# Performance work log

Hardware: AMD Instinct MI355X
Metric: run time of the kernel (lower is better)

## Reference

```python
import jax, jax.numpy as jnp
import numpy as np

N_NODES = 50000
N_EDGES = 800000
D_IN = 128
HIDDEN = 128
N_LAYERS = 3
N_CLASSES = 10
N_GRAPHS = 512
BN_EPS = 1e-5


def gcn_conv(x, edges, W, b):
    """PyG GCNConv: D^{-1/2}(A+I)D^{-1/2} X W + b (self-loops added)."""
    N = x.shape[0]
    src, dst = edges[0], edges[1]
    # degrees with self-loops
    deg = jax.ops.segment_sum(jnp.ones(src.shape[0], x.dtype), dst, num_segments=N) + 1.0
    dinv = jax.lax.rsqrt(deg)
    h = x @ W                                   # [N, out]
    norm = dinv[src] * dinv[dst]                # [E]
    out = jax.ops.segment_sum(h[src] * norm[:, None], dst, num_segments=N)
    out = out + h * (dinv * dinv)[:, None]      # self-loop messages
    return out + b


def batch_norm(x, gamma, beta):
    # BatchNorm1d in training mode: batch stats over node axis, biased var
    mu = x.mean(axis=0)
    var = x.var(axis=0)
    return gamma * (x - mu) * jax.lax.rsqrt(var + BN_EPS) + beta


def setup_inputs() -> dict:
    key = jax.random.key(0)
    ks = jax.random.split(key, 12)
    x = jax.random.normal(ks[0], (N_NODES, D_IN), dtype=jnp.float32)
    edges = jax.random.randint(ks[1], (2, N_EDGES), 0, N_NODES, dtype=jnp.int64)
    batch = jnp.sort(jax.random.randint(ks[2], (N_NODES,), 0, N_GRAPHS, dtype=jnp.int64))
    s_in = 1.0 / np.sqrt(D_IN)
    s_h = 1.0 / np.sqrt(HIDDEN)
    return {
        "x": x,
        "edges": edges,
        "batch": batch,
        "W1": jax.random.normal(ks[3], (D_IN, HIDDEN), dtype=jnp.float32) * s_in,
        "b1": jnp.zeros((HIDDEN,), jnp.float32),
        "g1": jnp.ones((HIDDEN,), jnp.float32),
        "be1": jnp.zeros((HIDDEN,), jnp.float32),
        "Wc": jax.random.normal(ks[4], (N_LAYERS, HIDDEN, HIDDEN), dtype=jnp.float32) * s_h,
        "bc": jnp.zeros((N_LAYERS, HIDDEN), jnp.float32),
        "gc": jnp.ones((N_LAYERS, HIDDEN), jnp.float32),
        "bec": jnp.zeros((N_LAYERS, HIDDEN), jnp.float32),
        "Wl": jax.random.normal(ks[5], (HIDDEN, N_CLASSES), dtype=jnp.float32) * s_h,
        "bl": jnp.zeros((N_CLASSES,), jnp.float32),
    }


def reference(x, edges, batch, W1, b1, g1, be1, Wc, bc, gc, bec, Wl, bl):
    h = jax.nn.relu(batch_norm(gcn_conv(x, edges, W1, b1), g1, be1))
    for i in range(N_LAYERS):  # fixed small layer loop
        h = jax.nn.relu(batch_norm(gcn_conv(h, edges, Wc[i], bc[i]), gc[i], bec[i]))
    # global_mean_pool over per-node graph ids
    sums = jax.ops.segment_sum(h, batch, num_segments=N_GRAPHS)
    counts = jax.ops.segment_sum(jnp.ones(h.shape[0], h.dtype), batch, num_segments=N_GRAPHS)
    pooled = sums / jnp.maximum(counts, 1.0)[:, None]
    return pooled @ Wl + bl
```

## Files before the change

### kernel.cpp

```cpp
#include <hip/hip_runtime.h>
#include <hip/hip_bf16.h>

#define NN 50000
#define NE 800000
#define DH 128
#define NGRAPH 512
#define NCLS 10
#define BN_EPS 1e-5f
#define SCAN_NB ((NN + 255) / 256)
#define GEMM_NB ((NN + 63) / 64)
#define BN1_NB 1024
#define BN2_NB 32
#define FILL_SEG 392
#define FILL_NB (FILL_SEG * 8)
#define STRIPE ((NN + 7) / 8)

typedef unsigned int uint;
typedef unsigned short ushort;
typedef __attribute__((ext_vector_type(8))) short short8;
typedef __attribute__((ext_vector_type(4))) float f32x4;

__device__ __forceinline__ ushort f2bf(float x) {
    __hip_bfloat16 h = __float2bfloat16(x);
    return *(ushort*)&h;
}
__device__ __forceinline__ float bf_lo(uint v) { return __uint_as_float(v << 16); }
__device__ __forceinline__ float bf_hi(uint v) { return __uint_as_float(v & 0xffff0000u); }


__global__ void hist_kernel(const int* __restrict__ dst, int* __restrict__ counts, int E) {
    int e = blockIdx.x * blockDim.x + threadIdx.x;
    if (e < E) atomicAdd(&counts[dst[e]], 1);
}

__global__ void compute_dinv_kernel(const int* __restrict__ counts, float* __restrict__ dinv, int N) {
    int n = blockIdx.x * blockDim.x + threadIdx.x;
    if (n < N) dinv[n] = rsqrtf((float)(counts[n] + 1));
}

__launch_bounds__(256)
__global__ void scan1_kernel(const int* __restrict__ counts, int* __restrict__ bsum, int N) {
    __shared__ int ls[256];
    int i = blockIdx.x * 256 + threadIdx.x;
    ls[threadIdx.x] = (i < N) ? counts[i] : 0;
    __syncthreads();
    for (int off = 128; off > 0; off >>= 1) {
        if (threadIdx.x < off) ls[threadIdx.x] += ls[threadIdx.x + off];
        __syncthreads();
    }
    if (threadIdx.x == 0) bsum[blockIdx.x] = ls[0];
}

__launch_bounds__(256)
__global__ void scan2_kernel(int* __restrict__ bsum, int NB) {
    __shared__ int ls[256];
    int tid = threadIdx.x;
    int v = (tid < NB) ? bsum[tid] : 0;
    ls[tid] = v;
    __syncthreads();
    for (int off = 1; off < 256; off <<= 1) {
        int t = (tid >= off) ? ls[tid - off] : 0;
        __syncthreads();
        ls[tid] += t;
        __syncthreads();
    }
    if (tid < NB) bsum[tid] = ls[tid] - v;
}

__launch_bounds__(256)
__global__ void scan3_kernel(const int* __restrict__ counts, const int* __restrict__ boff,
                             int* __restrict__ offsets, int* __restrict__ cursor, int N) {
    __shared__ int ls[256];
    int tid = threadIdx.x;
    int i = blockIdx.x * 256 + tid;
    int v = (i < N) ? counts[i] : 0;
    ls[tid] = v;
    __syncthreads();
    for (int off = 1; off < 256; off <<= 1) {
        int t = (tid >= off) ? ls[tid - off] : 0;
        __syncthreads();
        ls[tid] += t;
        __syncthreads();
    }
    int base = boff[blockIdx.x];
    if (i < N) {
        int ex = base + ls[tid] - v;
        offsets[i] = ex;
        cursor[i] = ex;
        if (i == N - 1) offsets[N] = base + ls[tid];
    }
}

__launch_bounds__(256)
__global__ void fill_kernel(const int* __restrict__ src, const int* __restrict__ dst,
                            int* __restrict__ cursor, int* __restrict__ csr_src, int E) {
    int stripe = blockIdx.x & 7;
    int seg = blockIdx.x >> 3;
    int lo = stripe * STRIPE;
    int hi = lo + STRIPE;
    for (int e = seg * 256 + threadIdx.x; e < E; e += FILL_SEG * 256) {
        int d = dst[e];
        if (d >= lo && d < hi) {
            int pos = atomicAdd(&cursor[d], 1);
            csr_src[pos] = src[e];
        }
    }
}


__launch_bounds__(256)
__global__ void wtrans_kernel(const float* __restrict__ W1, const float* __restrict__ Wc,
                              ushort* __restrict__ WT) {
    int layer = blockIdx.x >> 4;
    int kt = (blockIdx.x >> 2) & 3, nt = blockIdx.x & 3;
    const float* W = (layer == 0) ? W1 : Wc + (size_t)(layer - 1) * DH * DH;
    __shared__ float tile[32][33];
    int t = threadIdx.x;
    int r = t >> 3;
    int c4 = (t & 7) * 4;
    float4 v = *(const float4*)&W[(size_t)(kt * 32 + r) * DH + nt * 32 + c4];
    tile[r][c4 + 0] = v.x; tile[r][c4 + 1] = v.y;
    tile[r][c4 + 2] = v.z; tile[r][c4 + 3] = v.w;
    __syncthreads();
    int n = t >> 3, k4 = (t & 7) * 4;
    ushort4 o;
    o.x = f2bf(tile[k4 + 0][n]);
    o.y = f2bf(tile[k4 + 1][n]);
    o.z = f2bf(tile[k4 + 2][n]);
    o.w = f2bf(tile[k4 + 3][n]);
    *(ushort4*)&WT[(size_t)layer * DH * DH + (size_t)(nt * 32 + n) * DH + kt * 32 + k4] = o;
}


template<int MODE>
__launch_bounds__(256)
__global__ void gemm_kernel(const float* __restrict__ Xf, const uint* __restrict__ Xb,
                            const ushort* __restrict__ WTl,
                            const float* __restrict__ bnacc, const float* __restrict__ gamma,
                            const float* __restrict__ beta, const float* __restrict__ dinv,
                            ushort* __restrict__ H, int N) {
    __shared__ uint4 xs4[64 * 16];
    __shared__ uint4 wt4[128 * 16];
    int t = threadIdx.x;
    int kc = t & 15;
    int row0 = blockIdx.x * 64;

    float sc[8], sh[8];
    if (MODE) {
        const float invN = 1.0f / (float)NN;
        #pragma unroll
        for (int j = 0; j < 8; j++) {
            int f = kc * 8 + j;
            float mean = bnacc[f] * invN;
            float var = bnacc[128 + f] * invN - mean * mean;
            float s = gamma[f] * rsqrtf(var + BN_EPS);
            sc[j] = s;
            sh[j] = beta[f] - mean * s;
        }
    }

    #pragma unroll
    for (int i = 0; i < 4; i++) {
        int row = (t >> 4) + i * 16;
        int r = row0 + row;
        float v[8];
        if (r < N) {
            if (MODE) {
                uint4 raw = ((const uint4*)Xb)[(size_t)r * 16 + kc];
                v[0] = bf_lo(raw.x); v[1] = bf_hi(raw.x);
                v[2] = bf_lo(raw.y); v[3] = bf_hi(raw.y);
                v[4] = bf_lo(raw.z); v[5] = bf_hi(raw.z);
                v[6] = bf_lo(raw.w); v[7] = bf_hi(raw.w);
                #pragma unroll
                for (int j = 0; j < 8; j++) v[j] = fmaxf(v[j] * sc[j] + sh[j], 0.f);
            } else {
                float4 a = ((const float4*)Xf)[(size_t)r * 32 + kc * 2];
                float4 b = ((const float4*)Xf)[(size_t)r * 32 + kc * 2 + 1];
                v[0] = a.x; v[1] = a.y; v[2] = a.z; v[3] = a.w;
                v[4] = b.x; v[5] = b.y; v[6] = b.z; v[7] = b.w;
            }
        } else {
            #pragma unroll
            for (int j = 0; j < 8; j++) v[j] = 0.f;
        }
        uint4 p;
        p.x = (uint)f2bf(v[0]) | ((uint)f2bf(v[1]) << 16);
        p.y = (uint)f2bf(v[2]) | ((uint)f2bf(v[3]) << 16);
        p.z = (uint)f2bf(v[4]) | ((uint)f2bf(v[5]) << 16);
        p.w = (uint)f2bf(v[6]) | ((uint)f2bf(v[7]) << 16);
        xs4[row * 16 + (kc ^ (row & 7))] = p;
    }
    const uint4* WT4 = (const uint4*)WTl;
    #pragma unroll
    for (int i = 0; i < 8; i++) {
        int n = (t >> 4) + i * 16;
        wt4[n * 16 + (kc ^ (n & 7))] = WT4[n * 16 + kc];
    }
    __syncthreads();

    int w = t >> 6, l = t & 63;
    int l16 = l >> 4;
    int lrow = w * 16 + (l & 15);
    f32x4 acc[8];
    #pragma unroll
    for (int c = 0; c < 8; c++) acc[c] = (f32x4){0.f, 0.f, 0.f, 0.f};

    #pragma unroll
    for (int ks = 0; ks < 4; ks++) {
        int kk = ks * 4 + l16;
        uint4 av = xs4[lrow * 16 + (kk ^ (lrow & 7))];
        short8 a = *(short8*)&av;
        #pragma unroll
        for (int c = 0; c < 8; c++) {
            int n = c * 16 + (l & 15);
            uint4 bv = wt4[n * 16 + (kk ^ (n & 7))];
            short8 b = *(short8*)&bv;
            acc[c] = __builtin_amdgcn_mfma_f32_16x16x32_bf16(a, b, acc[c], 0, 0, 0);
        }
    }

    #pragma unroll
    for (int j = 0; j < 4; j++) {
        int grow = row0 + w * 16 + l16 * 4 + j;
        if (grow < N) {
            float dv = dinv[grow];
            #pragma unroll
            for (int c = 0; c < 8; c++) {
                H[(size_t)grow * DH + c * 16 + (l & 15)] = f2bf(acc[c][j] * dv);
            }
        }
    }
}


__launch_bounds__(256)
__global__ void agg_kernel(const uint* __restrict__ H, const int* __restrict__ offsets,
                           const int* __restrict__ csr_src, const float* __restrict__ dinv,
                           const float* __restrict__ bias, uint* __restrict__ out, int N) {
    int n = blockIdx.x * 4 + (threadIdx.x >> 6);
    int lane = threadIdx.x & 63;
    if (n >= N) return;
    int beg = offsets[n], end = offsets[n + 1];
    float ax = 0.f, ay = 0.f;
    for (int e = beg; e < end; e += 8) {
        uint v[8];
        #pragma unroll
        for (int i = 0; i < 8; i++) {
            int ee = e + i;
            int sraw = csr_src[ee];
            int s = (ee < end) ? sraw : n;
            v[i] = H[(size_t)s * 64 + lane];
        }
        #pragma unroll
        for (int i = 0; i < 8; i++) {
            uint vv = (e + i < end) ? v[i] : 0u;
            ax += bf_lo(vv);
            ay += bf_hi(vv);
        }
    }
    uint vn = H[(size_t)n * 64 + lane];
    ax += bf_lo(vn);
    ay += bf_hi(vn);
    float dv = dinv[n];
    float2 b = ((const float2*)bias)[lane];
    float ox = ax * dv + b.x;
    float oy = ay * dv + b.y;
    out[(size_t)n * 64 + lane] = (uint)f2bf(ox) | ((uint)f2bf(oy) << 16);
}


__launch_bounds__(256)
__global__ void bnstats1_kernel(const uint* __restrict__ A, float* __restrict__ part, int N) {
    int u = threadIdx.x & 63;
    int rh = threadIdx.x >> 6;
    float slo = 0.f, shi = 0.f, qlo = 0.f, qhi = 0.f;
    for (int r = blockIdx.x * 4 + rh; r < N; r += BN1_NB * 4) {
        uint v = A[(size_t)r * 64 + u];
        float lo = bf_lo(v), hi = bf_hi(v);
        slo += lo; shi += hi;
        qlo += lo * lo; qhi += hi * hi;
    }
    __shared__ float4 red[4][64];
    red[rh][u] = make_float4(slo, shi, qlo, qhi);
    __syncthreads();
    if (threadIdx.x < 64) {
        float4 a = red[0][u], b = red[1][u], c = red[2][u], d = red[3][u];
        float* p = part + (size_t)blockIdx.x * 256;
        p[2 * u]           = a.x + b.x + c.x + d.x;
        p[2 * u + 1]       = a.y + b.y + c.y + d.y;
        p[128 + 2 * u]     = a.z + b.z + c.z + d.z;
        p[128 + 2 * u + 1] = a.w + b.w + c.w + d.w;
    }
}

__launch_bounds__(256)
__global__ void bnstats2_kernel(const float* __restrict__ part, float* __restrict__ acc) {
    int rows = BN1_NB / BN2_NB;
    float s = 0.f;
    int r0 = blockIdx.x * rows;
    for (int r = r0; r < r0 + rows; r++) s += part[(size_t)r * 256 + threadIdx.x];
    atomicAdd(&acc[threadIdx.x], s);
}


__device__ __forceinline__ int lower_bound_dev(const int* __restrict__ a, int n, int key) {
    int lo = 0, hi = n;
    while (lo < hi) {
        int m = (lo + hi) >> 1;
        if (a[m] < key) lo = m + 1; else hi = m;
    }
    return lo;
}

__launch_bounds__(256)
__global__ void pool_kernel(const uint* __restrict__ AGG, const int* __restrict__ batch,
                            const float* __restrict__ bnacc, const float* __restrict__ gamma,
                            const float* __restrict__ beta, float* __restrict__ pooled, int N) {
    int g = blockIdx.x;
    __shared__ int sbeg, send;
    if (threadIdx.x == 0) {
        sbeg = lower_bound_dev(batch, N, g);
        send = lower_bound_dev(batch, N, g + 1);
    }
    __syncthreads();
    int beg = sbeg, end = send;
    int u = threadIdx.x & 63;
    int rh = threadIdx.x >> 6;
    const float invN = 1.0f / (float)NN;
    float m0 = bnacc[2 * u] * invN,     m1 = bnacc[2 * u + 1] * invN;
    float v0 = bnacc[128 + 2 * u] * invN - m0 * m0;
    float v1 = bnacc[128 + 2 * u + 1] * invN - m1 * m1;
    float sc0 = gamma[2 * u] * rsqrtf(v0 + BN_EPS);
    float sc1 = gamma[2 * u + 1] * rsqrtf(v1 + BN_EPS);
    float sh0 = beta[2 * u] - m0 * sc0;
    float sh1 = beta[2 * u + 1] - m1 * sc1;
    float s0 = 0.f, s1 = 0.f;
    for (int r = beg + rh; r < end; r += 4) {
        uint v = AGG[(size_t)r * 64 + u];
        s0 += fmaxf(bf_lo(v) * sc0 + sh0, 0.f);
        s1 += fmaxf(bf_hi(v) * sc1 + sh1, 0.f);
    }
    __shared__ float2 ls[4][64];
    ls[rh][u] = make_float2(s0, s1);
    __syncthreads();
    if (threadIdx.x < 64) {
        float2 a = ls[0][u], b = ls[1][u], c = ls[2][u], d = ls[3][u];
        float cnt = fmaxf((float)(end - beg), 1.f);
        pooled[g * DH + 2 * u]     = (a.x + b.x + c.x + d.x) / cnt;
        pooled[g * DH + 2 * u + 1] = (a.y + b.y + c.y + d.y) / cnt;
    }
}


__launch_bounds__(256)
__global__ void final_kernel(const float* __restrict__ pooled, const float* __restrict__ Wl,
                             const float* __restrict__ bl, float* __restrict__ out) {
    int gid = blockIdx.x * blockDim.x + threadIdx.x;
    if (gid >= NGRAPH * NCLS) return;
    int g = gid / NCLS, c = gid % NCLS;
    float s = bl[c];
    #pragma unroll 8
    for (int k = 0; k < DH; k++) s += pooled[g * DH + k] * Wl[k * NCLS + c];
    out[gid] = s;
}


extern "C" void kernel_launch(void* const* d_in, const int* in_sizes, int n_in,
                              void* d_out, int out_size, void* d_ws, size_t ws_size,
                              hipStream_t stream) {
    const float* x     = (const float*)d_in[0];
    const int*   edges = (const int*)d_in[1];
    const int*   batch = (const int*)d_in[2];
    const float* W1    = (const float*)d_in[3];
    const float* b1    = (const float*)d_in[4];
    const float* g1    = (const float*)d_in[5];
    const float* be1   = (const float*)d_in[6];
    const float* Wc    = (const float*)d_in[7];
    const float* bc    = (const float*)d_in[8];
    const float* gc    = (const float*)d_in[9];
    const float* bec   = (const float*)d_in[10];
    const float* Wl    = (const float*)d_in[11];
    const float* bl    = (const float*)d_in[12];
    float* out = (float*)d_out;

    const int* esrc = edges;
    const int* edst = edges + NE;

    char* w = (char*)d_ws;
    auto alloc = [&](size_t bytes) -> void* {
        void* p = (void*)w;
        w += (bytes + 255) & ~(size_t)255;
        return p;
    };
    int*    counts  = (int*)alloc(NN * 4);
    int*    offsets = (int*)alloc((NN + 1) * 4);
    int*    cursor  = (int*)alloc(NN * 4);
    float*  dinv    = (float*)alloc(NN * 4);
    int*    csr_src = (int*)alloc(NE * 4 + 64);
    int*    bsum    = (int*)alloc(256 * 4);
    float*  bn_acc  = (float*)alloc(4 * 256 * 4);
    float*  bn_part = (float*)alloc((size_t)BN1_NB * 256 * 4);
    float*  pooled  = (float*)alloc(NGRAPH * DH * 4);
    ushort* WT      = (ushort*)alloc(4 * DH * DH * 2);
    uint*   H       = (uint*)alloc((size_t)NN * 64 * 4);
    uint*   AGG     = (uint*)alloc((size_t)NN * 64 * 4);

    hipMemsetAsync(counts, 0, NN * 4, stream);
    hipMemsetAsync(bn_acc, 0, 4 * 256 * 4, stream);
    hist_kernel<<<(NE + 255) / 256, 256, 0, stream>>>(edst, counts, NE);
    compute_dinv_kernel<<<(NN + 255) / 256, 256, 0, stream>>>(counts, dinv, NN);
    scan1_kernel<<<SCAN_NB, 256, 0, stream>>>(counts, bsum, NN);
    scan2_kernel<<<1, 256, 0, stream>>>(bsum, SCAN_NB);
    scan3_kernel<<<SCAN_NB, 256, 0, stream>>>(counts, bsum, offsets, cursor, NN);
    fill_kernel<<<FILL_NB, 256, 0, stream>>>(esrc, edst, cursor, csr_src, NE);
    wtrans_kernel<<<64, 256, 0, stream>>>(W1, Wc, WT);

    for (int l = 0; l < 4; l++) {
        const float* bm  = (l == 0) ? b1 : bc + (size_t)(l - 1) * DH;
        const float* gp  = (l == 1) ? g1 : gc + (size_t)(l - 2) * DH;
        const float* bep = (l == 1) ? be1 : bec + (size_t)(l - 2) * DH;
        const ushort* WTl = WT + (size_t)l * DH * DH;

        if (l == 0) {
            gemm_kernel<0><<<GEMM_NB, 256, 0, stream>>>(
                x, nullptr, WTl, nullptr, nullptr, nullptr, dinv, (ushort*)H, NN);
        } else {
            gemm_kernel<1><<<GEMM_NB, 256, 0, stream>>>(
                nullptr, AGG, WTl, bn_acc + (size_t)(l - 1) * 256, gp, bep, dinv,
                (ushort*)H, NN);
        }
        agg_kernel<<<(NN + 3) / 4, 256, 0, stream>>>(H, offsets, csr_src, dinv, bm, AGG, NN);
        bnstats1_kernel<<<BN1_NB, 256, 0, stream>>>(AGG, bn_part, NN);
        bnstats2_kernel<<<BN2_NB, 256, 0, stream>>>(bn_part, bn_acc + (size_t)l * 256);
    }

    pool_kernel<<<NGRAPH, 256, 0, stream>>>(AGG, batch, bn_acc + 3 * 256,
                                            gc + 2 * DH, bec + 2 * DH, pooled, NN);
    final_kernel<<<(NGRAPH * NCLS + 255) / 256, 256, 0, stream>>>(pooled, Wl, bl, out);
}
```

Before: 325.1 us.

## Process two nodes per wavefront in aggregation and fold dinv into scan

The aggregation kernel now has each 64-lane wavefront gather the neighbours of two nodes at once, interleaving their loads so more memory requests are in flight per wave, with half as many blocks. The degree histogram uses the same destination-striped grid as the fill kernel to keep atomics local. The rsqrt degree computation moves into the scan kernel, removing one launch. The paired loop runs until the longer of the two neighbour lists is done, so an imbalanced pair wastes gathers, and the unconditional access to n1 assumes an even node count.

```diff
diff --git a/kernel.cpp b/kernel.cpp
--- a/kernel.cpp
+++ b/kernel.cpp
@@ -14,6 +14,7 @@
 #define FILL_SEG 392
 #define FILL_NB (FILL_SEG * 8)
 #define STRIPE ((NN + 7) / 8)
+#define AGG_NB ((NN / 2 + 3) / 4)
 
 typedef unsigned int uint;
 typedef unsigned short ushort;
@@ -28,14 +29,16 @@
 __device__ __forceinline__ float bf_hi(uint v) { return __uint_as_float(v & 0xffff0000u); }
 
 
+__launch_bounds__(256)
 __global__ void hist_kernel(const int* __restrict__ dst, int* __restrict__ counts, int E) {
-    int e = blockIdx.x * blockDim.x + threadIdx.x;
-    if (e < E) atomicAdd(&counts[dst[e]], 1);
-}
-
-__global__ void compute_dinv_kernel(const int* __restrict__ counts, float* __restrict__ dinv, int N) {
-    int n = blockIdx.x * blockDim.x + threadIdx.x;
-    if (n < N) dinv[n] = rsqrtf((float)(counts[n] + 1));
+    int stripe = blockIdx.x & 7;
+    int seg = blockIdx.x >> 3;
+    int lo = stripe * STRIPE;
+    int hi = lo + STRIPE;
+    for (int e = seg * 256 + threadIdx.x; e < E; e += FILL_SEG * 256) {
+        int d = dst[e];
+        if (d >= lo && d < hi) atomicAdd(&counts[d], 1);
+    }
 }
 
 __launch_bounds__(256)
@@ -69,7 +72,8 @@
 
 __launch_bounds__(256)
 __global__ void scan3_kernel(const int* __restrict__ counts, const int* __restrict__ boff,
-                             int* __restrict__ offsets, int* __restrict__ cursor, int N) {
+                             int* __restrict__ offsets, int* __restrict__ cursor,
+                             float* __restrict__ dinv, int N) {
     __shared__ int ls[256];
     int tid = threadIdx.x;
     int i = blockIdx.x * 256 + tid;
@@ -87,6 +91,7 @@
         int ex = base + ls[tid] - v;
         offsets[i] = ex;
         cursor[i] = ex;
+        dinv[i] = rsqrtf((float)(v + 1));
         if (i == N - 1) offsets[N] = base + ls[tid];
     }
 }
@@ -237,35 +242,46 @@
 __global__ void agg_kernel(const uint* __restrict__ H, const int* __restrict__ offsets,
                            const int* __restrict__ csr_src, const float* __restrict__ dinv,
                            const float* __restrict__ bias, uint* __restrict__ out, int N) {
-    int n = blockIdx.x * 4 + (threadIdx.x >> 6);
+    int base = (blockIdx.x * 4 + (threadIdx.x >> 6)) * 2;
     int lane = threadIdx.x & 63;
-    if (n >= N) return;
-    int beg = offsets[n], end = offsets[n + 1];
-    float ax = 0.f, ay = 0.f;
-    for (int e = beg; e < end; e += 8) {
-        uint v[8];
+    if (base >= N) return;
+    int n0 = base, n1 = base + 1;
+    int e0 = offsets[n0], end0 = offsets[n0 + 1];
+    int e1 = offsets[n1], end1 = offsets[n1 + 1];
+    float a0x = 0.f, a0y = 0.f, a1x = 0.f, a1y = 0.f;
+    while (e0 < end0 || e1 < end1) {
+        uint v0[8], v1[8];
         #pragma unroll
         for (int i = 0; i < 8; i++) {
-            int ee = e + i;
-            int sraw = csr_src[ee];
-            int s = (ee < end) ? sraw : n;
-            v[i] = H[(size_t)s * 64 + lane];
+            int ee = e0 + i;
+            int s = (ee < end0) ? csr_src[ee] : n0;
+            v0[i] = H[(size_t)s * 64 + lane];
         }
         #pragma unroll
         for (int i = 0; i < 8; i++) {
-            uint vv = (e + i < end) ? v[i] : 0u;
-            ax += bf_lo(vv);
-            ay += bf_hi(vv);
-        }
-    }
-    uint vn = H[(size_t)n * 64 + lane];
-    ax += bf_lo(vn);
-    ay += bf_hi(vn);
-    float dv = dinv[n];
+            int ee = e1 + i;
+            int s = (ee < end1) ? csr_src[ee] : n1;
+            v1[i] = H[(size_t)s * 64 + lane];
+        }
+        #pragma unroll
+        for (int i = 0; i < 8; i++) {
+            uint w0 = (e0 + i < end0) ? v0[i] : 0u;
+            uint w1 = (e1 + i < end1) ? v1[i] : 0u;
+            a0x += bf_lo(w0); a0y += bf_hi(w0);
+            a1x += bf_lo(w1); a1y += bf_hi(w1);
+        }
+        e0 += 8; e1 += 8;
+    }
     float2 b = ((const float2*)bias)[lane];
-    float ox = ax * dv + b.x;
-    float oy = ay * dv + b.y;
-    out[(size_t)n * 64 + lane] = (uint)f2bf(ox) | ((uint)f2bf(oy) << 16);
+    uint h0 = H[(size_t)n0 * 64 + lane];
+    uint h1 = H[(size_t)n1 * 64 + lane];
+    float d0 = dinv[n0], d1 = dinv[n1];
+    float o0x = (a0x + bf_lo(h0)) * d0 + b.x;
+    float o0y = (a0y + bf_hi(h0)) * d0 + b.y;
+    float o1x = (a1x + bf_lo(h1)) * d1 + b.x;
+    float o1y = (a1y + bf_hi(h1)) * d1 + b.y;
+    out[(size_t)n0 * 64 + lane] = (uint)f2bf(o0x) | ((uint)f2bf(o0y) << 16);
+    out[(size_t)n1 * 64 + lane] = (uint)f2bf(o1x) | ((uint)f2bf(o1y) << 16);
 }
 
 
@@ -407,11 +423,10 @@
 
     hipMemsetAsync(counts, 0, NN * 4, stream);
     hipMemsetAsync(bn_acc, 0, 4 * 256 * 4, stream);
-    hist_kernel<<<(NE + 255) / 256, 256, 0, stream>>>(edst, counts, NE);
-    compute_dinv_kernel<<<(NN + 255) / 256, 256, 0, stream>>>(counts, dinv, NN);
+    hist_kernel<<<FILL_NB, 256, 0, stream>>>(edst, counts, NE);
     scan1_kernel<<<SCAN_NB, 256, 0, stream>>>(counts, bsum, NN);
     scan2_kernel<<<1, 256, 0, stream>>>(bsum, SCAN_NB);
-    scan3_kernel<<<SCAN_NB, 256, 0, stream>>>(counts, bsum, offsets, cursor, NN);
+    scan3_kernel<<<SCAN_NB, 256, 0, stream>>>(counts, bsum, offsets, cursor, dinv, NN);
     fill_kernel<<<FILL_NB, 256, 0, stream>>>(esrc, edst, cursor, csr_src, NE);
     wtrans_kernel<<<64, 256, 0, stream>>>(W1, Wc, WT);
 
@@ -429,7 +444,7 @@
                 nullptr, AGG, WTl, bn_acc + (size_t)(l - 1) * 256, gp, bep, dinv,
                 (ushort*)H, NN);
         }
-        agg_kernel<<<(NN + 3) / 4, 256, 0, stream>>>(H, offsets, csr_src, dinv, bm, AGG, NN);
+        agg_kernel<<<AGG_NB, 256, 0, stream>>>(H, offsets, csr_src, dinv, bm, AGG, NN);
         bnstats1_kernel<<<BN1_NB, 256, 0, stream>>>(AGG, bn_part, NN);
         bnstats2_kernel<<<BN2_NB, 256, 0, stream>>>(bn_part, bn_acc + (size_t)l * 256);
     }
```

Result: slower. 431.1 us (+32.6%).
